# Kernel tuning notes

Hardware: AMD Instinct MI355X
Metric: run time of the kernel (lower is better)

Reference implementation:

```python
import jax, jax.numpy as jnp
import numpy as np
from jax import lax

B_SZ, SEQ, D_MODEL = 8, 2048, 1024
N_LAYER = 2
D_INNER = 2 * D_MODEL          # expand=2
D_STATE = 16
D_CONV = 4
DT_RANK = D_MODEL // 16        # ceil(1024/16)=64
EPS = 1e-5


def setup_inputs() -> dict:
    key = jax.random.key(0)
    ks = jax.random.split(key, 8)
    f = lambda k, shp, sc: jax.random.normal(k, shp, jnp.float32) * sc
    A_log = jnp.tile(jnp.log(jnp.arange(1, D_STATE + 1, dtype=jnp.float32)),
                     (N_LAYER, D_INNER, 1))  # S4D-real init, [L, d_inner, d_state]
    return {
        "x": f(ks[0], (B_SZ, SEQ, D_MODEL), 1.0),
        "in_proj_w": f(ks[1], (N_LAYER, 2 * D_INNER, D_MODEL), 0.02),
        "conv_w": f(ks[2], (N_LAYER, D_INNER, D_CONV), 0.2),
        "conv_b": jnp.zeros((N_LAYER, D_INNER), jnp.float32),
        "x_proj_w": f(ks[3], (N_LAYER, DT_RANK + 2 * D_STATE, D_INNER), 0.02),
        "dt_proj_w": f(ks[4], (N_LAYER, D_INNER, DT_RANK), 0.1),
        "dt_proj_b": f(ks[5], (N_LAYER, D_INNER), 0.5) - 4.0,  # softplus -> small dt
        "A_log": A_log,
        "D_param": jnp.ones((N_LAYER, D_INNER), jnp.float32),
        "out_proj_w": f(ks[6], (N_LAYER, D_MODEL, D_INNER), 0.02),
        "norm_w": jnp.ones((N_LAYER, D_MODEL), jnp.float32),
        "norm_b": jnp.zeros((N_LAYER, D_MODEL), jnp.float32),
    }


def _layer_norm(x, w, b):
    mu = jnp.mean(x, axis=-1, keepdims=True)
    var = jnp.mean(jnp.square(x - mu), axis=-1, keepdims=True)
    return (x - mu) * lax.rsqrt(var + EPS) * w + b


def _causal_dw_conv(x, w, b):
    # x: [B, Lq, d_inner], w: [d_inner, d_conv] depthwise causal conv
    xp = jnp.pad(x, ((0, 0), (D_CONV - 1, 0), (0, 0)))
    L = x.shape[1]
    y = b
    for k in range(D_CONV):
        y = y + xp[:, k:k + L, :] * w[:, k]
    return y


def _selective_scan(u, dt, Bm, Cm, A, Dp):
    # u, dt: [B, Lq, d_inner]; Bm, Cm: [B, Lq, d_state]; A: [d_inner, d_state]
    def step(h, inp):
        ut, dtt, Bt, Ct = inp                         # [B,di],[B,di],[B,ds],[B,ds]
        dA = jnp.exp(dtt[..., None] * A)              # [B, di, ds]
        h = dA * h + (dtt * ut)[..., None] * Bt[:, None, :]
        y = jnp.einsum('bds,bs->bd', h, Ct)
        return h, y

    h0 = jnp.zeros((u.shape[0], D_INNER, D_STATE), u.dtype)
    xs = (u.transpose(1, 0, 2), dt.transpose(1, 0, 2),
          Bm.transpose(1, 0, 2), Cm.transpose(1, 0, 2))
    _, ys = lax.scan(step, h0, xs)                    # ys: [Lq, B, di]
    return ys.transpose(1, 0, 2) + u * Dp


def _mamba(x, in_w, cw, cb, xpw, dtw, dtb, A_log, Dp, ow):
    xz = jnp.einsum('bld,ed->ble', x, in_w)           # [B, L, 2*d_inner]
    xi, z = jnp.split(xz, 2, axis=-1)
    xc = jax.nn.silu(_causal_dw_conv(xi, cw, cb))     # [B, L, d_inner]
    xdbl = jnp.einsum('bld,ed->ble', xc, xpw)         # [B, L, dt_rank+2*d_state]
    dt_low = xdbl[..., :DT_RANK]
    Bm = xdbl[..., DT_RANK:DT_RANK + D_STATE]
    Cm = xdbl[..., DT_RANK + D_STATE:]
    dt = jax.nn.softplus(jnp.einsum('blr,dr->bld', dt_low, dtw) + dtb)
    A = -jnp.exp(A_log)                               # [d_inner, d_state]
    y = _selective_scan(xc, dt, Bm, Cm, A, Dp)
    y = y * jax.nn.silu(z)
    return jnp.einsum('ble,de->bld', y, ow)           # [B, L, d_model]


def reference(x, in_proj_w, conv_w, conv_b, x_proj_w, dt_proj_w, dt_proj_b,
              A_log, D_param, out_proj_w, norm_w, norm_b):
    residual = None
    for l in range(N_LAYER):
        residual = x if residual is None else x + residual
        h = _layer_norm(residual, norm_w[l], norm_b[l])
        x = _mamba(h, in_proj_w[l], conv_w[l], conv_b[l], x_proj_w[l],
                   dt_proj_w[l], dt_proj_b[l], A_log[l], D_param[l], out_proj_w[l])
    # NOTE: source forward returns x without applying norm_f
    return x
```

## Files before the change

kernel.cpp:

```cpp
#include <hip/hip_runtime.h>
#include <cstddef>
#include <cstdint>

#define SEQB   8
#define SEQL   2048
#define DMODEL 1024
#define DINNER 2048
#define DSTATE 16
#define NC     32
#define TC     64
#define TT     8

typedef __attribute__((ext_vector_type(4))) float f32x4;
typedef __attribute__((ext_vector_type(8))) short bf16x8;
typedef unsigned int u32;
typedef const __attribute__((address_space(1))) u32* gas_ptr;
typedef __attribute__((address_space(3))) u32* las_ptr;

__device__ __forceinline__ void gld16(const void* g, void* l){
  __builtin_amdgcn_global_load_lds((gas_ptr)g, (las_ptr)l, 16, 0, 0);
}

__device__ __forceinline__ float siluf(float x){ return x / (1.f + __expf(-x)); }
__device__ __forceinline__ float softplusf(float x){ return (x > 20.f) ? x : log1pf(__expf(x)); }

__device__ __forceinline__ unsigned short f2bf_rne(float f){
  unsigned int u = __float_as_uint(f);
  u += 0x7FFFu + ((u>>16)&1u);
  return (unsigned short)(u>>16);
}
__device__ __forceinline__ void split_bf(float f, unsigned short& h, unsigned short& l){
  unsigned short hs = f2bf_rne(f);
  float hf = __uint_as_float(((unsigned int)hs)<<16);
  h = hs;
  l = f2bf_rne(f - hf);
}

#define CV8P(PH, PSRC) { \
  const float4* _p4 = (const float4*)(PSRC); \
  float4 _a = _p4[0], _b = _p4[1]; \
  bf16x8 _H, _L; unsigned short _h,_l; \
  split_bf(_a.x,_h,_l); _H[0]=(short)_h; _L[0]=(short)_l; \
  split_bf(_a.y,_h,_l); _H[1]=(short)_h; _L[1]=(short)_l; \
  split_bf(_a.z,_h,_l); _H[2]=(short)_h; _L[2]=(short)_l; \
  split_bf(_a.w,_h,_l); _H[3]=(short)_h; _L[3]=(short)_l; \
  split_bf(_b.x,_h,_l); _H[4]=(short)_h; _L[4]=(short)_l; \
  split_bf(_b.y,_h,_l); _H[5]=(short)_h; _L[5]=(short)_l; \
  split_bf(_b.z,_h,_l); _H[6]=(short)_h; _L[6]=(short)_l; \
  split_bf(_b.w,_h,_l); _H[7]=(short)_h; _L[7]=(short)_l; \
  *(bf16x8*)(PH) = _H; *(bf16x8*)((unsigned short*)(PH) + 64) = _L; }

__global__ __launch_bounds__(256)
void wsplit2(const float* __restrict__ src, unsigned short* __restrict__ dst,
             int K, int k4shift)
{
  int idx = blockIdx.x*256 + threadIdx.x;
  int r  = idx >> k4shift;
  int c4 = idx & ((1<<k4shift)-1);
  float4 v = ((const float4*)src)[idx];
  unsigned short h,l; short4 h4, l4;
  split_bf(v.x,h,l); h4.x=(short)h; l4.x=(short)l;
  split_bf(v.y,h,l); h4.y=(short)h; l4.y=(short)l;
  split_bf(v.z,h,l); h4.z=(short)h; l4.z=(short)l;
  split_bf(v.w,h,l); h4.w=(short)h; l4.w=(short)l;
  size_t ro = (size_t)r*2*K;
  *(short4*)&dst[ro + (c4<<2)]     = h4;
  *(short4*)&dst[ro + K + (c4<<2)] = l4;
}

__global__ __launch_bounds__(256)
void wsplit_og(const float* __restrict__ src, unsigned short* __restrict__ dst)
{
  int idx = blockIdx.x*256 + threadIdx.x;
  int r  = idx >> 9;
  int c4 = idx & 511;
  int layer = r >> 10, rr = r & 1023;
  float4 v = ((const float4*)src)[idx];
  unsigned short h,l; short4 h4, l4;
  split_bf(v.x,h,l); h4.x=(short)h; l4.x=(short)l;
  split_bf(v.y,h,l); h4.y=(short)h; l4.y=(short)l;
  split_bf(v.z,h,l); h4.z=(short)h; l4.z=(short)l;
  split_bf(v.w,h,l); h4.w=(short)h; l4.w=(short)l;
  int col = c4 << 2;
  int g = col >> 8, j = col & 255;
  size_t base = (size_t)layer*1024*4096 + (size_t)rr*4096 + g*512 + j;
  *(short4*)&dst[base]       = h4;
  *(short4*)&dst[base + 256] = l4;
}

__global__ __launch_bounds__(256)
void ln_split2(const float* __restrict__ a, const float* __restrict__ res,
               const float* __restrict__ w, const float* __restrict__ bias,
               unsigned short* __restrict__ Hs)
{
  int row = blockIdx.x;
  size_t off = (size_t)row * DMODEL;
  float4 v = ((const float4*)(a + off))[threadIdx.x];
  if (res){
    float4 u = ((const float4*)(res + off))[threadIdx.x];
    v.x += u.x; v.y += u.y; v.z += u.z; v.w += u.w;
  }
  float s  = v.x + v.y + v.z + v.w;
  float s2 = fmaf(v.x,v.x, fmaf(v.y,v.y, fmaf(v.z,v.z, v.w*v.w)));
  #pragma unroll
  for (int o=32;o>0;o>>=1){ s += __shfl_down(s,o,64); s2 += __shfl_down(s2,o,64); }
  __shared__ float red[8];
  int lane = threadIdx.x & 63, wid = threadIdx.x >> 6;
  if (lane==0){ red[wid]=s; red[4+wid]=s2; }
  __syncthreads();
  s  = red[0]+red[1]+red[2]+red[3];
  s2 = red[4]+red[5]+red[6]+red[7];
  float mu  = s * (1.f/DMODEL);
  float var = s2 * (1.f/DMODEL) - mu*mu;
  float rstd = rsqrtf(var + 1e-5f);
  float4 wv = ((const float4*)w)[threadIdx.x];
  float4 bv = ((const float4*)bias)[threadIdx.x];
  float4 o4;
  o4.x = (v.x-mu)*rstd*wv.x + bv.x;
  o4.y = (v.y-mu)*rstd*wv.y + bv.y;
  o4.z = (v.z-mu)*rstd*wv.z + bv.z;
  o4.w = (v.w-mu)*rstd*wv.w + bv.w;
  unsigned short h,l; short4 h4, l4;
  split_bf(o4.x,h,l); h4.x=(short)h; l4.x=(short)l;
  split_bf(o4.y,h,l); h4.y=(short)h; l4.y=(short)l;
  split_bf(o4.z,h,l); h4.z=(short)h; l4.z=(short)l;
  split_bf(o4.w,h,l); h4.w=(short)h; l4.w=(short)l;
  size_t ro = (size_t)row*2048;
  int c = threadIdx.x<<2;
  *(short4*)&Hs[ro + c]        = h4;
  *(short4*)&Hs[ro + 1024 + c] = l4;
}

__global__ __launch_bounds__(256)
void mgemm_in(const unsigned short* __restrict__ A,
              const unsigned short* __restrict__ B,
              float* __restrict__ XI, float* __restrict__ ZB)
{
  __shared__ __align__(16) unsigned short As[2][128*64];
  __shared__ __align__(16) unsigned short Bs[2][128*64];
  const int t = threadIdx.x;
  const int mbase = blockIdx.y << 7, nbase = blockIdx.x << 7;

  const int lane = t & 63, w = t >> 6;
  const int wr = w >> 1, wc = w & 1;
  const int l16 = lane & 15, kq = lane >> 4;

  const int sr8 = lane >> 3, sl8 = lane & 7;
  const unsigned short* pA[4]; const unsigned short* pB[4];
  int dofs[4];
  #pragma unroll
  for (int c=0;c<4;c++){
    int row = c*32 + w*8 + sr8;
    int ss  = sl8 ^ (row & 7);
    int colb = (ss < 4) ? (ss<<3) : (1024 + ((ss-4)<<3));
    pA[c] = A + (size_t)(mbase+row)*2048 + colb;
    pB[c] = B + (size_t)(nbase+row)*2048 + colb;
    dofs[c] = row*64 + sl8*8;
  }

  f32x4 acc[4][4];
  #pragma unroll
  for (int i=0;i<4;i++)
    #pragma unroll
    for (int j=0;j<4;j++) acc[i][j] = (f32x4){0.f,0.f,0.f,0.f};

#define STG(buf, k0) { _Pragma("unroll") \
    for (int c=0;c<4;c++){ \
      gld16(pA[c] + (k0), &As[buf][dofs[c]]); \
      gld16(pB[c] + (k0), &Bs[buf][dofs[c]]); \
    } }

  STG(0, 0);
  asm volatile("s_waitcnt vmcnt(0)" ::: "memory");
  __builtin_amdgcn_s_barrier();
  __builtin_amdgcn_sched_barrier(0);

  for (int i=0; i<32; i++){
    const int cur = i & 1, nxt = cur ^ 1;
    const bool hn = (i+1 < 32);
    if (hn){
      STG(nxt, (i+1)*32);
      asm volatile("s_waitcnt vmcnt(8)" ::: "memory");
    } else {
      asm volatile("s_waitcnt vmcnt(0)" ::: "memory");
    }
    __builtin_amdgcn_s_barrier();
    __builtin_amdgcn_sched_barrier(0);

    const unsigned short* Ac = As[cur];
    const unsigned short* Bc = Bs[cur];
    bf16x8 ah[4], al[4];
    #pragma unroll
    for (int mf=0; mf<4; mf++){
      int ra = wr*64 + mf*16 + l16;
      ah[mf] = *(const bf16x8*)&Ac[ra*64 + (( kq      ^ (ra&7))<<3)];
      al[mf] = *(const bf16x8*)&Ac[ra*64 + (((kq+4)   ^ (ra&7))<<3)];
    }
    #pragma unroll
    for (int nf=0; nf<4; nf++){
      int rb = wc*64 + nf*16 + l16;
      bf16x8 bh = *(const bf16x8*)&Bc[rb*64 + (( kq    ^ (rb&7))<<3)];
      bf16x8 bl = *(const bf16x8*)&Bc[rb*64 + (((kq+4) ^ (rb&7))<<3)];
      #pragma unroll
      for (int mf=0; mf<4; mf++){
        acc[mf][nf] = __builtin_amdgcn_mfma_f32_16x16x32_bf16(ah[mf], bh, acc[mf][nf], 0,0,0);
        acc[mf][nf] = __builtin_amdgcn_mfma_f32_16x16x32_bf16(ah[mf], bl, acc[mf][nf], 0,0,0);
        acc[mf][nf] = __builtin_amdgcn_mfma_f32_16x16x32_bf16(al[mf], bh, acc[mf][nf], 0,0,0);
      }
    }
    __builtin_amdgcn_s_barrier();
  }
#undef STG

  float* Cd = (nbase < 2048) ? XI : ZB;
  const int cb = (nbase < 2048) ? nbase : (nbase - 2048);
  #pragma unroll
  for (int mf=0; mf<4; mf++){
    int r0 = mbase + wr*64 + mf*16 + kq*4;
    #pragma unroll
    for (int nf=0; nf<4; nf++){
      int c = cb + wc*64 + nf*16 + l16;
      #pragma unroll
      for (int r=0;r<4;r++)
        Cd[(size_t)(r0+r)*2048 + c] = acc[mf][nf][r];
    }
  }
}

__global__ __launch_bounds__(256)
void mgemm_out3(const unsigned short* __restrict__ A,
                const unsigned short* __restrict__ B,
                float* __restrict__ C)
{
  __shared__ __align__(16) unsigned short As[2][128*64];
  __shared__ __align__(16) unsigned short Bs[2][128*64];
  const int t = threadIdx.x;
  const int mbase = blockIdx.y << 7, nbase = blockIdx.x << 7;

  const int lane = t & 63, w = t >> 6;
  const int wr = w >> 1, wc = w & 1;
  const int l16 = lane & 15, kq = lane >> 4;

  const int sr8 = lane >> 3, sl8 = lane & 7;
  const unsigned short* pA[4]; const unsigned short* pB[4];
  int dofs[4];
  #pragma unroll
  for (int c=0;c<4;c++){
    int row = c*32 + w*8 + sr8;
    int ss  = sl8 ^ (row & 7);
    int pofs = (ss < 4) ? (ss<<3) : (256 + ((ss-4)<<3));
    pA[c] = A + (size_t)(mbase+row)*4096 + pofs;
    pB[c] = B + (size_t)(nbase+row)*4096 + pofs;
    dofs[c] = row*64 + sl8*8;
  }

  f32x4 acc[4][4];
  #pragma unroll
  for (int i=0;i<4;i++)
    #pragma unroll
    for (int j=0;j<4;j++) acc[i][j] = (f32x4){0.f,0.f,0.f,0.f};

#define GSO(i) ((((i)*32)>>8)<<9) + (((i)*32) & 255)
#define STG(buf, i) { const int gso = GSO(i); _Pragma("unroll") \
    for (int c=0;c<4;c++){ \
      gld16(pA[c] + gso, &As[buf][dofs[c]]); \
      gld16(pB[c] + gso, &Bs[buf][dofs[c]]); \
    } }

  STG(0, 0);
  asm volatile("s_waitcnt vmcnt(0)" ::: "memory");
  __builtin_amdgcn_s_barrier();
  __builtin_amdgcn_sched_barrier(0);

  for (int i=0; i<64; i++){
    const int cur = i & 1, nxt = cur ^ 1;
    const bool hn = (i+1 < 64);
    if (hn){
      STG(nxt, i+1);
      asm volatile("s_waitcnt vmcnt(8)" ::: "memory");
    } else {
      asm volatile("s_waitcnt vmcnt(0)" ::: "memory");
    }
    __builtin_amdgcn_s_barrier();
    __builtin_amdgcn_sched_barrier(0);

    const unsigned short* Ac = As[cur];
    const unsigned short* Bc = Bs[cur];
    bf16x8 ah[4], al[4];
    #pragma unroll
    for (int mf=0; mf<4; mf++){
      int ra = wr*64 + mf*16 + l16;
      ah[mf] = *(const bf16x8*)&Ac[ra*64 + (( kq      ^ (ra&7))<<3)];
      al[mf] = *(const bf16x8*)&Ac[ra*64 + (((kq+4)   ^ (ra&7))<<3)];
    }
    #pragma unroll
    for (int nf=0; nf<4; nf++){
      int rb = wc*64 + nf*16 + l16;
      bf16x8 bh = *(const bf16x8*)&Bc[rb*64 + (( kq    ^ (rb&7))<<3)];
      bf16x8 bl = *(const bf16x8*)&Bc[rb*64 + (((kq+4) ^ (rb&7))<<3)];
      #pragma unroll
      for (int mf=0; mf<4; mf++){
        acc[mf][nf] = __builtin_amdgcn_mfma_f32_16x16x32_bf16(ah[mf], bh, acc[mf][nf], 0,0,0);
        acc[mf][nf] = __builtin_amdgcn_mfma_f32_16x16x32_bf16(ah[mf], bl, acc[mf][nf], 0,0,0);
        acc[mf][nf] = __builtin_amdgcn_mfma_f32_16x16x32_bf16(al[mf], bh, acc[mf][nf], 0,0,0);
      }
    }
    __builtin_amdgcn_s_barrier();
  }
#undef STG
#undef GSO

  #pragma unroll
  for (int mf=0; mf<4; mf++){
    int r0 = mbase + wr*64 + mf*16 + kq*4;
    #pragma unroll
    for (int nf=0; nf<4; nf++){
      int c = nbase + wc*64 + nf*16 + l16;
      #pragma unroll
      for (int r=0;r<4;r++)
        C[(size_t)(r0+r)*1024 + c] = acc[mf][nf][r];
    }
  }
}

__global__ __launch_bounds__(256)
void xproj_pair(const unsigned short* __restrict__ A,
                const unsigned short* __restrict__ W2,
                float* __restrict__ XD)
{
  __shared__ __align__(16) unsigned short S[2][128*64];
  const int t = threadIdx.x;
  const int mbase = blockIdx.x << 5;
  const int lane = t & 63, w = t >> 6;
  const int mf = w & 1, nc0 = (w >> 1) * 48;
  const int l16 = lane & 15, kq = lane >> 4;

  const unsigned short* ps[4]; int dofs[4];
  #pragma unroll
  for (int c=0;c<4;c++){
    int idx = c*256 + t;
    int row = idx >> 3, sl8 = idx & 7;
    int ss  = sl8 ^ (row & 7);
    int colb = (ss < 4) ? (ss<<3) : (2048 + ((ss-4)<<3));
    ps[c] = (row < 32) ? (A + (size_t)(mbase+row)*4096 + colb)
                       : (W2 + (size_t)(row-32)*4096 + colb);
    dofs[c] = row*64 + sl8*8;
  }

  f32x4 acc[3];
  #pragma unroll
  for (int j=0;j<3;j++) acc[j] = (f32x4){0.f,0.f,0.f,0.f};

#define STG(buf, k0) { _Pragma("unroll") \
    for (int c=0;c<4;c++) gld16(ps[c] + (k0), &S[buf][dofs[c]]); }

  STG(0, 0);
  asm volatile("s_waitcnt vmcnt(0)" ::: "memory");
  __builtin_amdgcn_s_barrier();
  __builtin_amdgcn_sched_barrier(0);

  for (int i=0; i<64; i++){
    const int cur = i & 1, nxt = cur ^ 1;
    const bool hn = (i+1 < 64);
    if (hn){
      STG(nxt, (i+1)*32);
      asm volatile("s_waitcnt vmcnt(4)" ::: "memory");
    } else {
      asm volatile("s_waitcnt vmcnt(0)" ::: "memory");
    }
    __builtin_amdgcn_s_barrier();
    __builtin_amdgcn_sched_barrier(0);

    const unsigned short* Sc = S[cur];
    int ra = mf*16 + l16;
    bf16x8 ah = *(const bf16x8*)&Sc[ra*64 + (( kq    ^ (ra&7))<<3)];
    bf16x8 al = *(const bf16x8*)&Sc[ra*64 + (((kq+4) ^ (ra&7))<<3)];
    #pragma unroll
    for (int nf=0; nf<3; nf++){
      int rb = 32 + nc0 + nf*16 + l16;
      bf16x8 bh = *(const bf16x8*)&Sc[rb*64 + (( kq    ^ (rb&7))<<3)];
      bf16x8 bl = *(const bf16x8*)&Sc[rb*64 + (((kq+4) ^ (rb&7))<<3)];
      acc[nf] = __builtin_amdgcn_mfma_f32_16x16x32_bf16(ah, bh, acc[nf], 0,0,0);
      acc[nf] = __builtin_amdgcn_mfma_f32_16x16x32_bf16(ah, bl, acc[nf], 0,0,0);
      acc[nf] = __builtin_amdgcn_mfma_f32_16x16x32_bf16(al, bh, acc[nf], 0,0,0);
    }
    __builtin_amdgcn_s_barrier();
  }
#undef STG

  #pragma unroll
  for (int nf=0; nf<3; nf++){
    int c = nc0 + nf*16 + l16;
    int r0s = mbase + mf*16 + kq*4;
    #pragma unroll
    for (int r=0;r<4;r++)
      XD[(size_t)(r0s+r)*96 + c] = acc[nf][r];
  }
}

__global__ __launch_bounds__(256)
void mgemm_dt2(const float* __restrict__ XDf,
               const unsigned short* __restrict__ DTW2,
               float* __restrict__ XI,
               const float* __restrict__ dtb)
{
  __shared__ __align__(16) unsigned short As[128*128];
  __shared__ __align__(16) unsigned short Bs[128*128];
  const int t = threadIdx.x;
  const int mbase = blockIdx.y << 7, nbase = blockIdx.x << 7;
  const int lane = t & 63, w = t >> 6;
  const int wr = w >> 1, wc = w & 1;
  const int l16 = lane & 15, kq = lane >> 4;

  {
    const int row = t >> 1, half = (t & 1) << 5;
    const int r7 = row & 7;
    const float* src = XDf + (size_t)(mbase + row)*96 + half;
    #pragma unroll
    for (int i=0;i<4;i++){
      int g = (half >> 3) + i;
      CV8P(&As[row*128 + ((g ^ r7)<<3)], src + i*8);
    }
  }
  {
    #pragma unroll
    for (int q=0;q<8;q++){
      int idx = q*256 + t;
      int row = idx >> 4, sl = idx & 15;
      int ss  = (sl & 8) | ((sl & 7) ^ (row & 7));
      int col = (ss < 8) ? (ss<<3) : (64 + ((ss-8)<<3));
      gld16(DTW2 + (size_t)(nbase+row)*128 + col, &Bs[row*128 + sl*8]);
    }
  }
  __syncthreads();

  f32x4 acc[4][4];
  #pragma unroll
  for (int i=0;i<4;i++)
    #pragma unroll
    for (int j=0;j<4;j++) acc[i][j] = (f32x4){0.f,0.f,0.f,0.f};

  #pragma unroll
  for (int kb=0; kb<3; kb++){
    const int aoff = (kb==2) ? 8 : 0;
    const int boff = (kb==1) ? 8 : 0;
    #pragma unroll
    for (int kw=0; kw<2; kw++){
      const int sbase = kw*4 + kq;
      bf16x8 af[4];
      #pragma unroll
      for (int mf=0; mf<4; mf++){
        int ra = wr*64 + mf*16 + l16;
        int sA = ((sbase ^ (ra&7)) + aoff);
        af[mf] = *(const bf16x8*)&As[ra*128 + (sA<<3)];
      }
      #pragma unroll
      for (int nf=0; nf<4; nf++){
        int rb = wc*64 + nf*16 + l16;
        int sB = ((sbase ^ (rb&7)) + boff);
        bf16x8 bfr = *(const bf16x8*)&Bs[rb*128 + (sB<<3)];
        #pragma unroll
        for (int mf=0; mf<4; mf++)
          acc[mf][nf] = __builtin_amdgcn_mfma_f32_16x16x32_bf16(af[mf], bfr, acc[mf][nf], 0,0,0);
      }
    }
  }

  #pragma unroll
  for (int mf=0; mf<4; mf++){
    int r0 = mbase + wr*64 + mf*16 + kq*4;
    #pragma unroll
    for (int nf=0; nf<4; nf++){
      int c = nbase + wc*64 + nf*16 + l16;
      float eb = dtb[c];
      #pragma unroll
      for (int r=0;r<4;r++)
        XI[(size_t)(r0+r)*2048 + c] = softplusf(acc[mf][nf][r] + eb);
    }
  }
}

__global__ __launch_bounds__(256)
void conv_silu4(const float* __restrict__ xi, const float* __restrict__ cw,
                const float* __restrict__ cb, unsigned short* __restrict__ u2)
{
  const int r0 = blockIdx.x << 2;
  const int d0 = threadIdx.x << 3;
  const int tt0 = r0 & (SEQL-1);

  float wk[4][8];
  {
    const float4* cw4 = (const float4*)(cw + (size_t)d0*4);
    #pragma unroll
    for (int j=0;j<8;j++){
      float4 wj = cw4[j];
      wk[0][j]=wj.x; wk[1][j]=wj.y; wk[2][j]=wj.z; wk[3][j]=wj.w;
    }
  }
  float bias[8];
  *(float4*)&bias[0] = *(const float4*)(cb + d0);
  *(float4*)&bias[4] = *(const float4*)(cb + d0 + 4);

  float v[7][8];
#define LD8(dst, p) { *(float4*)&dst[0] = ((const float4*)(p))[0]; \
                      *(float4*)&dst[4] = ((const float4*)(p))[1]; }
  #pragma unroll
  for (int k=0;k<7;k++){
    int trel = tt0 - 3 + k;
    if (trel >= 0){
      LD8(v[k], xi + (size_t)(r0 - 3 + k)*DINNER + d0);
    } else {
      #pragma unroll
      for (int j=0;j<8;j++) v[k][j] = 0.f;
    }
  }
#undef LD8

  #pragma unroll
  for (int jrow=0; jrow<4; jrow++){
    unsigned short h8[8], l8[8];
    #pragma unroll
    for (int j=0;j<8;j++){
      float y = fmaf(v[jrow+3][j], wk[3][j], fmaf(v[jrow+2][j], wk[2][j],
                fmaf(v[jrow+1][j], wk[1][j], fmaf(v[jrow][j], wk[0][j], bias[j]))));
      float uv = siluf(y);
      split_bf(uv, h8[j], l8[j]);
    }
    unsigned short* outp = u2 + (size_t)(r0 + jrow)*4096 + d0;
    *(uint4*)outp          = *(const uint4*)h8;
    *(uint4*)(outp + 2048) = *(const uint4*)l8;
  }
}

template<int PASS>
__global__ __launch_bounds__(256)
void scan_chunk(const unsigned short* __restrict__ u2, float* __restrict__ dty,
                const float* __restrict__ xdbl, const float* __restrict__ zb,
                const float* __restrict__ A_log, const float* __restrict__ Dp,
                float* __restrict__ hfin, float* __restrict__ sumdt)
{
  __shared__ __align__(16) float Tdt[2][TT][256];
  __shared__ __align__(16) float Tu [2][TT][256];
  __shared__ __align__(16) float Tz [(PASS==3)?2:1][(PASS==3)?TT:1][(PASS==3)?256:4];
  __shared__ __align__(16) float Tbc[2][TT][32];

  const int tid = threadIdx.x;
  const int idx = blockIdx.x*256 + tid;
  const int d = idx & (DINNER-1);
  const int g = idx >> 11;
  const int cck = g & (NC-1);
  const int bb = g >> 5;
  const int wv = tid >> 6, ln = tid & 63;
  const int dbase = (blockIdx.x << 8) & (DINNER-1);

  float A2[16];
  {
    const float* al = A_log + (size_t)d*DSTATE;
    #pragma unroll
    for (int s=0;s<16;s++) A2[s] = -expf(al[s]) * 1.44269504f;
  }
  float h[16];
  if (PASS == 1){
    #pragma unroll
    for (int s=0;s<16;s++) h[s] = 0.f;
  } else {
    const float* hp = hfin + ((size_t)g*DINNER + d)*16;
    #pragma unroll
    for (int s=0;s<16;s+=4) *(float4*)&h[s] = *(const float4*)(hp + s);
  }
  const float Dv = (PASS==3) ? Dp[d] : 0.f;

  const size_t row0 = (size_t)bb*SEQL + (size_t)cck*TC;

#define STAGE(buf, T0) do { \
    _Pragma("unroll") \
    for (int q=0;q<2;q++){ \
      int r = q*4 + wv; \
      size_t rowi = row0 + (T0) + r; \
      gld16(dty + rowi*2048 + dbase + ln*4, &Tdt[buf][r][0]); \
      const unsigned short* us = u2 + rowi*4096 + \
          ((ln < 32) ? (dbase + ln*8) : (2048 + dbase + (ln-32)*8)); \
      gld16(us, &Tu[buf][r][0]); \
      if (PASS==3) gld16(zb + rowi*2048 + dbase + ln*4, &Tz[buf][r][0]); \
    } \
    if (wv == 3){ \
      gld16(xdbl + (row0 + (T0) + (ln>>3))*96 + 64 + (ln&7)*4, &Tbc[buf][0][0]); \
    } \
  } while(0)

  STAGE(0, 0);
  asm volatile("s_waitcnt vmcnt(0)" ::: "memory");
  __builtin_amdgcn_s_barrier();
  __builtin_amdgcn_sched_barrier(0);

  float sdt = 0.f;

  for (int t0 = 0; t0 < TC; t0 += TT){
    const int cur = (t0 >> 3) & 1, nxt = cur ^ 1;
    const bool hasNext = (t0 + TT < TC);
    if (hasNext) STAGE(nxt, t0 + TT);

    if (hasNext){
      if (PASS==3){
        if (wv==3) asm volatile("s_waitcnt vmcnt(7)" ::: "memory");
        else       asm volatile("s_waitcnt vmcnt(6)" ::: "memory");
      } else {
        if (wv==3) asm volatile("s_waitcnt vmcnt(5)" ::: "memory");
        else       asm volatile("s_waitcnt vmcnt(4)" ::: "memory");
      }
    } else {
      asm volatile("s_waitcnt vmcnt(0)" ::: "memory");
    }
    __builtin_amdgcn_s_barrier();
    __builtin_amdgcn_sched_barrier(0);

    #pragma unroll
    for (int tt=0; tt<TT; tt++){
      float dtc = Tdt[cur][tt][tid];
      const unsigned short* tur = (const unsigned short*)&Tu[cur][tt][0];
      float uc = __uint_as_float((u32)tur[tid] << 16)
               + __uint_as_float((u32)tur[256+tid] << 16);
      float Bv[16], Cv[16];
      #pragma unroll
      for (int q=0;q<4;q++) *(float4*)&Bv[q*4] = *(const float4*)&Tbc[cur][tt][q*4];
      if (PASS==3){
        #pragma unroll
        for (int q=0;q<4;q++) *(float4*)&Cv[q*4] = *(const float4*)&Tbc[cur][tt][16+q*4];
      }
      if (PASS==1) sdt += dtc;
      float du = dtc*uc;
      float y = 0.f;
      #pragma unroll
      for (int s=0;s<16;s++){
        float dA = exp2f(dtc*A2[s]);
        h[s] = fmaf(dA, h[s], du*Bv[s]);
        if (PASS==3) y = fmaf(h[s], Cv[s], y);
      }
      if (PASS==3){
        float zc = Tz[cur][tt][tid];
        y = fmaf(uc, Dv, y);
        float gv = y * siluf(zc);
        unsigned short gh, gl;
        split_bf(gv, gh, gl);
        Tdt[cur][tt][tid] = __uint_as_float((u32)gh | ((u32)gl << 16));
      }
    }

    if (PASS==3) asm volatile("s_waitcnt lgkmcnt(0)" ::: "memory");
    __builtin_amdgcn_s_barrier();
    __builtin_amdgcn_sched_barrier(0);

    if (PASS==3){
      #pragma unroll
      for (int q=0;q<2;q++){
        int r = q*4 + wv;
        size_t rowi = row0 + t0 + r;
        const u32* T = (const u32*)&Tdt[cur][r][0];
        int o0 = ln*4;
        u32 vals[4];
        if (ln < 32){
          #pragma unroll
          for (int k=0;k<4;k++){
            int i2 = (o0+k)*2;
            vals[k] = (T[i2] & 0xFFFFu) | (T[i2+1] << 16);
          }
        } else {
          #pragma unroll
          for (int k=0;k<4;k++){
            int i2 = (o0+k-128)*2;
            vals[k] = (T[i2] >> 16) | (T[i2+1] & 0xFFFF0000u);
          }
        }
        *(float4*)(dty + rowi*2048 + dbase + o0) = *(const float4*)vals;
      }
    }
  }
#undef STAGE

  if (PASS==1){
    float* hp = hfin + ((size_t)g*DINNER + d)*16;
    #pragma unroll
    for (int s=0;s<16;s+=4) *(float4*)(hp + s) = *(const float4*)&h[s];
    sumdt[(size_t)g*DINNER + d] = sdt;
  }
}

__global__ __launch_bounds__(256)
void scan_prop(const float* __restrict__ A_log, float* __restrict__ hfin,
               const float* __restrict__ sumdt)
{
  int idx = blockIdx.x*256 + threadIdx.x;
  int s = idx & 15;
  int d = (idx >> 4) & (DINNER-1);
  int b = idx >> 15;
  float A2 = -expf(A_log[(size_t)d*DSTATE + s]) * 1.44269504f;
  float H = 0.f;
  size_t hbase = ((size_t)b*NC*DINNER + d)*16 + s;
  size_t sbase = (size_t)b*NC*DINNER + d;
  for (int c=0;c<NC;c++){
    float P   = exp2f(A2 * sumdt[sbase + (size_t)c*DINNER]);
    float tmp = hfin[hbase + (size_t)c*DINNER*16];
    hfin[hbase + (size_t)c*DINNER*16] = H;
    H = fmaf(P, H, tmp);
  }
}

extern "C" void kernel_launch(void* const* d_in, const int* in_sizes, int n_in,
                              void* d_out, int out_size, void* d_ws, size_t ws_size,
                              hipStream_t stream)
{
  const float* x    = (const float*)d_in[0];
  const float* in_w = (const float*)d_in[1];
  const float* cw   = (const float*)d_in[2];
  const float* cb   = (const float*)d_in[3];
  const float* xpw  = (const float*)d_in[4];
  const float* dtw  = (const float*)d_in[5];
  const float* dtb  = (const float*)d_in[6];
  const float* A_log= (const float*)d_in[7];
  const float* Dp   = (const float*)d_in[8];
  const float* ow   = (const float*)d_in[9];
  const float* nw   = (const float*)d_in[10];
  const float* nb   = (const float*)d_in[11];
  float* outF = (float*)d_out;

  const size_t fixedB = 33554432ULL + 16777216ULL + 1572864ULL + 1048576ULL;
  const size_t perB   = 58720256ULL;
  int NB = 4;
  while (NB > 1 && fixedB + (size_t)NB*perB > ws_size) NB >>= 1;
  const int Mc = NB * SEQL;
  const int nchunk = SEQB / NB;

  unsigned short* INW2  = (unsigned short*)d_ws;
  unsigned short* OUTWG = INW2 + (size_t)2*4096*2048;
  unsigned short* XPW2  = OUTWG + (size_t)2*1024*4096;
  unsigned short* DTW2  = XPW2 + (size_t)2*96*4096;
  char* dyn = (char*)(DTW2 + (size_t)2*2048*128);

  unsigned short* SH = (unsigned short*)dyn;
  float* XD = (float*)dyn;
  float* HF = (float*)(dyn + (size_t)Mc*384);
  float* SD = (float*)(dyn + (size_t)Mc*2432);
  float* XI = (float*)(dyn + (size_t)Mc*4096);
  float* ZB = XI + (size_t)Mc*2048;
  unsigned short* U2 = (unsigned short*)(ZB + (size_t)Mc*2048);

  wsplit2<<<8192, 256, 0, stream>>>(in_w, INW2, 1024, 8);
  wsplit2<<<384,  256, 0, stream>>>(xpw,  XPW2, 2048, 9);
  wsplit2<<<256,  256, 0, stream>>>(dtw,  DTW2, 64, 4);
  wsplit_og<<<4096, 256, 0, stream>>>(ow, OUTWG);

  for (int c = 0; c < nchunk; ++c){
    const size_t rowoff = (size_t)c * Mc;
    const float* xrows = x + rowoff * DMODEL;
    float* X1 = outF + rowoff * DMODEL;

    for (int l = 0; l < 2; ++l){
      const float* Al = A_log + (size_t)l*DINNER*DSTATE;

      ln_split2<<<Mc, 256, 0, stream>>>(
          (l==0) ? xrows : X1, (l==0) ? nullptr : xrows,
          nw + (size_t)l*DMODEL, nb + (size_t)l*DMODEL, SH);

      mgemm_in<<<dim3(32, Mc/128), 256, 0, stream>>>(
          SH, INW2 + (size_t)l*4096*2048, XI, ZB);

      conv_silu4<<<Mc/4, 256, 0, stream>>>(
          XI, cw + (size_t)l*DINNER*4, cb + (size_t)l*DINNER, U2);

      xproj_pair<<<Mc/32, 256, 0, stream>>>(
          U2, XPW2 + (size_t)l*96*4096, XD);

      mgemm_dt2<<<dim3(16, Mc/128), 256, 0, stream>>>(
          XD, DTW2 + (size_t)l*2048*128, XI, dtb + (size_t)l*DINNER);

      scan_chunk<1><<<NB*NC*8, 256, 0, stream>>>(
          U2, XI, XD, ZB, Al, Dp + (size_t)l*DINNER, HF, SD);
      scan_prop<<<NB*128, 256, 0, stream>>>(Al, HF, SD);
      scan_chunk<3><<<NB*NC*8, 256, 0, stream>>>(
          U2, XI, XD, ZB, Al, Dp + (size_t)l*DINNER, HF, SD);

      mgemm_out3<<<dim3(8, Mc/128), 256, 0, stream>>>(
          (const unsigned short*)XI, OUTWG + (size_t)l*1024*4096, X1);
    }
  }
}
```

Before: 3.055 ms.

## Enlarge in-projection GEMM tile to 256x256 with 8 waves, single-buffered LDS

```diff
diff --git a/kernel.cpp b/kernel.cpp
--- a/kernel.cpp
+++ b/kernel.cpp
@@ -131,18 +131,17 @@
   *(short4*)&Hs[ro + 1024 + c] = l4;
 }
 
-__global__ __launch_bounds__(256)
-void mgemm_in(const unsigned short* __restrict__ A,
-              const unsigned short* __restrict__ B,
-              float* __restrict__ XI, float* __restrict__ ZB)
-{
-  __shared__ __align__(16) unsigned short As[2][128*64];
-  __shared__ __align__(16) unsigned short Bs[2][128*64];
+__global__ __launch_bounds__(512)
+void mgemm_in8(const unsigned short* __restrict__ A,
+               const unsigned short* __restrict__ B,
+               float* __restrict__ XI, float* __restrict__ ZB)
+{
+  __shared__ __align__(16) unsigned short As[256*64];
+  __shared__ __align__(16) unsigned short Bs[256*64];
   const int t = threadIdx.x;
-  const int mbase = blockIdx.y << 7, nbase = blockIdx.x << 7;
-
+  const int mbase = blockIdx.y << 8, nbase = blockIdx.x << 8;
   const int lane = t & 63, w = t >> 6;
-  const int wr = w >> 1, wc = w & 1;
+  const int wr = w & 3, wc = w >> 2;
   const int l16 = lane & 15, kq = lane >> 4;
 
   const int sr8 = lane >> 3, sl8 = lane & 7;
@@ -150,7 +149,7 @@
   int dofs[4];
   #pragma unroll
   for (int c=0;c<4;c++){
-    int row = c*32 + w*8 + sr8;
+    int row = w*32 + c*8 + sr8;
     int ss  = sl8 ^ (row & 7);
     int colb = (ss < 4) ? (ss<<3) : (1024 + ((ss-4)<<3));
     pA[c] = A + (size_t)(mbase+row)*2048 + colb;
@@ -158,49 +157,31 @@
     dofs[c] = row*64 + sl8*8;
   }
 
-  f32x4 acc[4][4];
+  f32x4 acc[4][8];
   #pragma unroll
   for (int i=0;i<4;i++)
     #pragma unroll
-    for (int j=0;j<4;j++) acc[i][j] = (f32x4){0.f,0.f,0.f,0.f};
-
-#define STG(buf, k0) { _Pragma("unroll") \
-    for (int c=0;c<4;c++){ \
-      gld16(pA[c] + (k0), &As[buf][dofs[c]]); \
-      gld16(pB[c] + (k0), &Bs[buf][dofs[c]]); \
-    } }
-
-  STG(0, 0);
-  asm volatile("s_waitcnt vmcnt(0)" ::: "memory");
-  __builtin_amdgcn_s_barrier();
-  __builtin_amdgcn_sched_barrier(0);
-
-  for (int i=0; i<32; i++){
-    const int cur = i & 1, nxt = cur ^ 1;
-    const bool hn = (i+1 < 32);
-    if (hn){
-      STG(nxt, (i+1)*32);
-      asm volatile("s_waitcnt vmcnt(8)" ::: "memory");
-    } else {
-      asm volatile("s_waitcnt vmcnt(0)" ::: "memory");
-    }
-    __builtin_amdgcn_s_barrier();
-    __builtin_amdgcn_sched_barrier(0);
-
-    const unsigned short* Ac = As[cur];
-    const unsigned short* Bc = Bs[cur];
+    for (int j=0;j<8;j++) acc[i][j] = (f32x4){0.f,0.f,0.f,0.f};
+
+  for (int k0=0; k0<1024; k0+=32){
+    #pragma unroll
+    for (int c=0;c<4;c++){
+      gld16(pA[c] + k0, &As[dofs[c]]);
+      gld16(pB[c] + k0, &Bs[dofs[c]]);
+    }
+    __syncthreads();
     bf16x8 ah[4], al[4];
     #pragma unroll
     for (int mf=0; mf<4; mf++){
       int ra = wr*64 + mf*16 + l16;
-      ah[mf] = *(const bf16x8*)&Ac[ra*64 + (( kq      ^ (ra&7))<<3)];
-      al[mf] = *(const bf16x8*)&Ac[ra*64 + (((kq+4)   ^ (ra&7))<<3)];
-    }
-    #pragma unroll
-    for (int nf=0; nf<4; nf++){
-      int rb = wc*64 + nf*16 + l16;
-      bf16x8 bh = *(const bf16x8*)&Bc[rb*64 + (( kq    ^ (rb&7))<<3)];
-      bf16x8 bl = *(const bf16x8*)&Bc[rb*64 + (((kq+4) ^ (rb&7))<<3)];
+      ah[mf] = *(const bf16x8*)&As[ra*64 + (( kq      ^ (ra&7))<<3)];
+      al[mf] = *(const bf16x8*)&As[ra*64 + (((kq+4)   ^ (ra&7))<<3)];
+    }
+    #pragma unroll
+    for (int nf=0; nf<8; nf++){
+      int rb = wc*128 + nf*16 + l16;
+      bf16x8 bh = *(const bf16x8*)&Bs[rb*64 + (( kq    ^ (rb&7))<<3)];
+      bf16x8 bl = *(const bf16x8*)&Bs[rb*64 + (((kq+4) ^ (rb&7))<<3)];
       #pragma unroll
       for (int mf=0; mf<4; mf++){
         acc[mf][nf] = __builtin_amdgcn_mfma_f32_16x16x32_bf16(ah[mf], bh, acc[mf][nf], 0,0,0);
@@ -208,9 +189,8 @@
         acc[mf][nf] = __builtin_amdgcn_mfma_f32_16x16x32_bf16(al[mf], bh, acc[mf][nf], 0,0,0);
       }
     }
-    __builtin_amdgcn_s_barrier();
-  }
-#undef STG
+    __syncthreads();
+  }
 
   float* Cd = (nbase < 2048) ? XI : ZB;
   const int cb = (nbase < 2048) ? nbase : (nbase - 2048);
@@ -218,8 +198,8 @@
   for (int mf=0; mf<4; mf++){
     int r0 = mbase + wr*64 + mf*16 + kq*4;
     #pragma unroll
-    for (int nf=0; nf<4; nf++){
-      int c = cb + wc*64 + nf*16 + l16;
+    for (int nf=0; nf<8; nf++){
+      int c = cb + wc*128 + nf*16 + l16;
       #pragma unroll
       for (int r=0;r<4;r++)
         Cd[(size_t)(r0+r)*2048 + c] = acc[mf][nf][r];
@@ -761,7 +741,7 @@
           (l==0) ? xrows : X1, (l==0) ? nullptr : xrows,
           nw + (size_t)l*DMODEL, nb + (size_t)l*DMODEL, SH);
 
-      mgemm_in<<<dim3(32, Mc/128), 256, 0, stream>>>(
+      mgemm_in8<<<dim3(16, Mc/256), 512, 0, stream>>>(
           SH, INW2 + (size_t)l*4096*2048, XI, ZB);
 
       conv_silu4<<<Mc/4, 256, 0, stream>>>(
```

Result: no change. 2.996 ms, median of 3 (-1.9%).
